# Performance work log

Measured on AMD Instinct MI355X. Metric: run time of the kernel, lower is better.

Reference implementation:

```python
import jax, jax.numpy as jnp
import numpy as np

N = 100_000      # nodes
E = 1_600_000    # edges (avg degree 16)
H = 4            # heads
C = 32           # per-head channels
HID = 128        # hidden = H*C
L = 4            # layers
IN, ED, OUT = 8, 6, 256
NEG_SLOPE = 0.2  # LeakyReLU default in GATv2Conv


def setup_inputs() -> dict:
    key = jax.random.key(0)
    ks = jax.random.split(key, 16)
    s = 0.1
    return {
        "x": jax.random.normal(ks[0], (N, IN), dtype=jnp.float32),
        "edge_index": jax.random.randint(ks[1], (2, E), 0, N, dtype=jnp.int32),
        "edge_attr": jax.random.normal(ks[2], (E, ED), dtype=jnp.float32),
        "W_in": jax.random.normal(ks[3], (IN, HID), dtype=jnp.float32) * s,
        "b_in": jnp.zeros((HID,), jnp.float32),
        "W_l": jax.random.normal(ks[4], (L, HID, HID), dtype=jnp.float32) * s,
        "b_l": jnp.zeros((L, HID), jnp.float32),
        "W_r": jax.random.normal(ks[5], (L, HID, HID), dtype=jnp.float32) * s,
        "b_r": jnp.zeros((L, HID), jnp.float32),
        "W_e": jax.random.normal(ks[6], (L, ED, HID), dtype=jnp.float32) * s,
        "att": jax.random.normal(ks[7], (L, H, C), dtype=jnp.float32) * s,
        "bias": jnp.zeros((L, HID), jnp.float32),
        "ln_w": jnp.ones((L, HID), jnp.float32),
        "ln_b": jnp.zeros((L, HID), jnp.float32),
        "W_out": jax.random.normal(ks[8], (HID, OUT), dtype=jnp.float32) * s,
        "b_out": jnp.zeros((OUT,), jnp.float32),
    }


def _elu(x):
    return jnp.where(x > 0, x, jnp.expm1(x))


def _leaky(x):
    return jnp.where(x > 0, x, NEG_SLOPE * x)


def _layernorm(x, w, b):
    mu = jnp.mean(x, axis=-1, keepdims=True)
    var = jnp.var(x, axis=-1, keepdims=True)
    return (x - mu) * jax.lax.rsqrt(var + 1e-5) * w + b


def _forward(x, edge_index, edge_attr, W_in, b_in, W_l, b_l, W_r, b_r,
             W_e, att, bias, ln_w, ln_b, W_out, b_out):
    src, dst = edge_index[0], edge_index[1]
    # add_self_loops with fill_value='mean': self-loop edge_attr = mean of incoming edge_attr
    deg = jax.ops.segment_sum(jnp.ones((E,), x.dtype), dst, num_segments=N)
    loop_attr = jax.ops.segment_sum(edge_attr, dst, num_segments=N) / jnp.maximum(deg, 1.0)[:, None]
    loops = jnp.arange(N, dtype=src.dtype)
    src_a = jnp.concatenate([src, loops])          # [E+N]
    dst_a = jnp.concatenate([dst, loops])          # [E+N]
    eattr_a = jnp.concatenate([edge_attr, loop_attr], axis=0)  # [E+N, ED]

    h = _elu(x @ W_in + b_in)  # [N, HID]
    for i in range(L):
        res = h
        xl = (h @ W_l[i] + b_l[i]).reshape(N, H, C)   # source transform
        xr = (h @ W_r[i] + b_r[i]).reshape(N, H, C)   # target transform
        ea = (eattr_a @ W_e[i]).reshape(-1, H, C)     # edge transform
        m = _leaky(xl[src_a] + xr[dst_a] + ea)        # [E+N, H, C]
        score = jnp.einsum('ehc,hc->eh', m, att[i])   # [E+N, H]
        # segment softmax over incoming edges per target node
        smax = jax.ops.segment_max(score, dst_a, num_segments=N)[dst_a]
        ex = jnp.exp(score - smax)
        denom = jax.ops.segment_sum(ex, dst_a, num_segments=N)[dst_a]
        alpha = ex / denom                             # [E+N, H]
        out = jax.ops.segment_sum(alpha[:, :, None] * xl[src_a], dst_a,
                                  num_segments=N).reshape(N, HID) + bias[i]
        h = _elu(_layernorm(out + res, ln_w[i], ln_b[i]))
        # dropout: identity (eval mode)
    return h @ W_out + b_out  # [N, OUT]


def reference(x, edge_index, edge_attr, W_in, b_in, W_l, b_l, W_r, b_r,
              W_e, att, bias, ln_w, ln_b, W_out, b_out):
    return _forward(x, edge_index, edge_attr, W_in, b_in, W_l, b_l, W_r, b_r,
                    W_e, att, bias, ln_w, ln_b, W_out, b_out)
```

## Files before the change

kernel.cpp:

```cpp
#include <hip/hip_runtime.h>
#include <hip/hip_bf16.h>
#include <hip/hip_fp16.h>

#define N_NODES 100000
#define N_EDGES 1600000
#define HEADS 4
#define CHN 32
#define HID 128
#define LAYERS 4
#define IN_F 8
#define ED_F 6
#define OUT_F 256
#define NEG_SLOPE 0.2f

typedef _Float16 f16x8 __attribute__((ext_vector_type(8)));
typedef _Float16 f16x4 __attribute__((ext_vector_type(4)));
typedef _Float16 h2 __attribute__((ext_vector_type(2)));
typedef float f32x4 __attribute__((ext_vector_type(4)));

#if defined(__has_builtin)
#if __has_builtin(__builtin_amdgcn_fdot2)
#define HAVE_FDOT2 1
#endif
#endif

__device__ __forceinline__ float elu_f(float x) {
    return x > 0.f ? x : expm1f(x);
}

__device__ __forceinline__ h2 bith2(float f) {
    union { float f; h2 h; } u; u.f = f; return u.h;
}

__device__ __forceinline__ float dot6(h2 e01, h2 e23, h2 e45, const h2* w) {
#ifdef HAVE_FDOT2
    return __builtin_amdgcn_fdot2(e45, w[2],
           __builtin_amdgcn_fdot2(e23, w[1],
           __builtin_amdgcn_fdot2(e01, w[0], 0.f, false), false), false);
#else
    float s = (float)e01[0] * (float)w[0][0];
    s = fmaf((float)e01[1], (float)w[0][1], s);
    s = fmaf((float)e23[0], (float)w[1][0], s);
    s = fmaf((float)e23[1], (float)w[1][1], s);
    s = fmaf((float)e45[0], (float)w[2][0], s);
    s = fmaf((float)e45[1], (float)w[2][1], s);
    return s;
#endif
}


__global__ void hist_kernel(const int* __restrict__ dst, int* __restrict__ fill) {
    int e = blockIdx.x * blockDim.x + threadIdx.x;
    if (e < N_EDGES) atomicAdd(&fill[dst[e]], 1);
}

__global__ void scan1_kernel(const int* __restrict__ cnt, int* __restrict__ bsum) {
    __shared__ int sd[256];
    int t = threadIdx.x;
    int base = blockIdx.x * 1024 + t * 4;
    int s = 0;
#pragma unroll
    for (int j = 0; j < 4; ++j) {
        int i = base + j;
        if (i < N_NODES) s += cnt[i];
    }
    sd[t] = s;
    for (int off = 128; off > 0; off >>= 1) {
        __syncthreads();
        if (t < off) sd[t] += sd[t + off];
    }
    if (t == 0) bsum[blockIdx.x] = sd[0];
}

__global__ void scan2_kernel(int* __restrict__ bsum, int* __restrict__ rowptr, int nb) {
    __shared__ int sd[256];
    int t = threadIdx.x;
    int v = (t < nb) ? bsum[t] : 0;
    sd[t] = v;
    __syncthreads();
    for (int off = 1; off < 256; off <<= 1) {
        int x = (t >= off) ? sd[t - off] : 0;
        __syncthreads();
        sd[t] += x;
        __syncthreads();
    }
    if (t < nb) bsum[t] = sd[t] - v;
    if (t == 0) rowptr[N_NODES] = sd[255];
}

__global__ void scan3_kernel(const int* __restrict__ cnt, const int* __restrict__ bsum,
                             int* __restrict__ rowptr) {
    __shared__ int sd[256];
    int t = threadIdx.x;
    int base = blockIdx.x * 1024 + t * 4;
    int v[4];
#pragma unroll
    for (int j = 0; j < 4; ++j) {
        int i = base + j;
        v[j] = (i < N_NODES) ? cnt[i] : 0;
    }
    int s = v[0] + v[1] + v[2] + v[3];
    sd[t] = s;
    __syncthreads();
    for (int off = 1; off < 256; off <<= 1) {
        int xv = (t >= off) ? sd[t - off] : 0;
        __syncthreads();
        sd[t] += xv;
        __syncthreads();
    }
    int excl = sd[t] - s + bsum[blockIdx.x];
    int pre = 0;
#pragma unroll
    for (int j = 0; j < 4; ++j) {
        int i = base + j;
        if (i < N_NODES) rowptr[i] = excl + pre;
        pre += v[j];
    }
}

__global__ void fill_kernel(const int* __restrict__ src, const int* __restrict__ dst,
                            const int* __restrict__ rowptr, int* __restrict__ fill,
                            int2* __restrict__ csr) {
    int e = blockIdx.x * blockDim.x + threadIdx.x;
    if (e >= N_EDGES) return;
    int d = dst[e];
    int p = rowptr[d] + atomicAdd(&fill[d], 1);
    csr[p] = make_int2(src[e] * (HID * 2), e * 16);
}

__global__ void ecvt_kernel(const float* __restrict__ eattr, __half* __restrict__ ea16) {
    int gid = blockIdx.x * blockDim.x + threadIdx.x;
    if (gid >= N_EDGES * 8) return;
    int e = gid >> 3, d = gid & 7;
    float v = (d < ED_F) ? eattr[e * ED_F + d] : 0.f;
    ea16[gid] = __float2half_rn(v);
}

__global__ void lattr_kernel(const int* __restrict__ rowptr, const int2* __restrict__ csr,
                             const float* __restrict__ eattr, __half* __restrict__ lat16) {
    int gid = blockIdx.x * blockDim.x + threadIdx.x;
    if (gid >= N_NODES * 8) return;
    int n = gid >> 3;
    int d = gid & 7;
    float s = 0.f;
    if (d < ED_F) {
        int rp0 = rowptr[n], rp1 = rowptr[n + 1];
        for (int p = rp0; p < rp1; ++p) {
            int eid = csr[p].y >> 4;
            s += eattr[(size_t)eid * ED_F + d];
        }
        int deg = rp1 - rp0;
        s /= (float)(deg > 0 ? deg : 1);
    }
    lat16[gid] = __float2half_rn(s);
}


__global__ void convw_kernel(const float* __restrict__ W_l, const float* __restrict__ W_r,
                             const float* __restrict__ W_out, __half* __restrict__ wbt) {
    int gid = blockIdx.x * blockDim.x + threadIdx.x;
    if (gid >= 5 * 256 * 128) return;
    int b = gid >> 15;
    int idx = gid & 32767;
    int n = idx >> 7, k = idx & 127;
    float val;
    if (b < 4)
        val = (n < HID) ? W_l[b * HID * HID + k * HID + n]
                        : W_r[b * HID * HID + k * HID + (n - HID)];
    else
        val = W_out[k * OUT_F + n];
    int boff = n * 256 + ((k * 2) ^ ((n & 7) << 4));
    *(__half*)((char*)wbt + (size_t)b * 65536 + boff) = __float2half_rn(val);
}


__global__ void in_kernel(const float* __restrict__ x, const float* __restrict__ Wi,
                          const float* __restrict__ bi, __half* __restrict__ h16) {
    int gid = blockIdx.x * blockDim.x + threadIdx.x;
    if (gid >= N_NODES * HID) return;
    int n = gid >> 7, j = gid & 127;
    float acc = bi[j];
#pragma unroll
    for (int k = 0; k < IN_F; ++k) acc = fmaf(x[n * IN_F + k], Wi[k * HID + j], acc);
    h16[gid] = __float2half_rn(elu_f(acc));
}


#define LDS_B_OFF 16384

template <int MODE>
__global__ __launch_bounds__(256, 2) void gemm_kernel(
    const __half* __restrict__ A16, const __half* __restrict__ Bt,
    const float* __restrict__ bias0, const float* __restrict__ bias1,
    __half* __restrict__ xl16, float* __restrict__ xr_out, float* __restrict__ outp) {
    __shared__ __align__(16) unsigned char smem[81920];
    int t = threadIdx.x;
    int row0 = blockIdx.x * 64;

#pragma unroll
    for (int it = 0; it < 4; ++it) {
        int idx = it * 256 + t;
        int r = idx >> 4;
        int kb = (idx & 15) * 16;
        f16x8 p = *(const f16x8*)((const char*)A16 + (size_t)(row0 + r) * 256 + kb);
        *(f16x8*)(smem + r * 256 + (kb ^ ((r & 7) << 4))) = p;
    }
#pragma unroll
    for (int it = 0; it < 16; ++it) {
        int off = (it * 256 + t) * 16;
        *(float4*)(smem + LDS_B_OFF + off) = *(const float4*)((const char*)Bt + off);
    }
    __syncthreads();

    int wave = t >> 6;
    int lane = t & 63;
    int lc = lane & 15, lr = lane >> 4;
    int cbase = wave * 64;

    f32x4 acc[4][4];
#pragma unroll
    for (int i = 0; i < 4; ++i)
#pragma unroll
        for (int j = 0; j < 4; ++j) acc[i][j] = (f32x4){0.f, 0.f, 0.f, 0.f};

#pragma unroll
    for (int kk = 0; kk < 4; ++kk) {
        int kb = kk * 64 + lr * 16;
        f16x8 av[4], bv[4];
#pragma unroll
        for (int rt = 0; rt < 4; ++rt) {
            int r = rt * 16 + lc;
            av[rt] = *(const f16x8*)(smem + r * 256 + (kb ^ ((r & 7) << 4)));
        }
#pragma unroll
        for (int ct = 0; ct < 4; ++ct) {
            int c = cbase + ct * 16 + lc;
            bv[ct] = *(const f16x8*)(smem + LDS_B_OFF + c * 256 + (kb ^ ((c & 7) << 4)));
        }
#pragma unroll
        for (int rt = 0; rt < 4; ++rt)
#pragma unroll
            for (int ct = 0; ct < 4; ++ct)
                acc[rt][ct] = __builtin_amdgcn_mfma_f32_16x16x32_f16(av[rt], bv[ct],
                                                                     acc[rt][ct], 0, 0, 0);
    }

#pragma unroll
    for (int ct = 0; ct < 4; ++ct) {
        int col = cbase + ct * 16 + lc;
        float bv;
        if (MODE == 0) bv = (col < HID) ? bias0[col] : bias1[col - HID];
        else bv = bias0[col];
#pragma unroll
        for (int rt = 0; rt < 4; ++rt) {
#pragma unroll
            for (int q = 0; q < 4; ++q) {
                int node = row0 + rt * 16 + lr * 4 + q;
                if (node < N_NODES) {
                    float val = acc[rt][ct][q] + bv;
                    if (MODE == 0) {
                        if (col < HID)
                            xl16[(size_t)node * HID + col] = __float2half_rn(val);
                        else
                            xr_out[(size_t)node * HID + (col - HID)] = val;
                    } else {
                        outp[(size_t)node * OUT_F + col] = val;
                    }
                }
            }
        }
    }
}


struct Slot {
    float4 er;
    float2 xv;
};

__device__ __forceinline__ void slot_issue(Slot& s, int i, int total, int rp0,
                                           const int2* __restrict__ csr,
                                           const char* eab, const char* lat16v,
                                           const char* xlb, int vbytes) {
    i = min(i, total - 1);
    const char* eb;
    const char* xb;
    if (i == 0) {
        eb = lat16v;
        xb = xlb + (size_t)vbytes;
    } else {
        int2 se = csr[rp0 + i - 1];
        eb = eab + (size_t)se.y;
        xb = xlb + (size_t)se.x;
    }
    s.er = *(const float4*)eb;
    s.xv = *(const float2*)xb;
}

__device__ __forceinline__ void slot_consume(const Slot& sl, int i, int total,
                                             const h2 we_h2[4][3], const float* attv,
                                             const float* xrv,
                                             float& denom, float* acc) {
    h2 e01 = bith2(sl.er.x), e23 = bith2(sl.er.y), e45 = bith2(sl.er.z);
    h2 x01 = bith2(sl.xv.x), x23 = bith2(sl.xv.y);
    float xf[4];
    xf[0] = (float)x01[0]; xf[1] = (float)x01[1];
    xf[2] = (float)x23[0]; xf[3] = (float)x23[1];
    float t = 0.f;
#pragma unroll
    for (int c = 0; c < 4; ++c) {
        float ea = dot6(e01, e23, e45, we_h2[c]);
        float m = xf[c] + xrv[c] + ea;
        m = m > 0.f ? m : NEG_SLOPE * m;
        t = fmaf(m, attv[c], t);
    }
    t += __shfl_xor(t, 1);
    t += __shfl_xor(t, 2);
    t += __shfl_xor(t, 4);
    float ex = __expf(t);
    ex = (i < total) ? ex : 0.f;
    denom += ex;
#pragma unroll
    for (int c = 0; c < 4; ++c) acc[c] = fmaf(ex, xf[c], acc[c]);
}

__global__ __launch_bounds__(64, 8) void edge_kernel(
    const __half* __restrict__ xl, const float* __restrict__ xr,
    __half* __restrict__ h16,
    const int* __restrict__ rowptr, const int2* __restrict__ csr,
    const __half* __restrict__ ea16, const __half* __restrict__ lat16,
    const float* __restrict__ We, const float* __restrict__ att,
    const float* __restrict__ bias_l, const float* __restrict__ lnw,
    const float* __restrict__ lnb) {
    int v = blockIdx.x;
    int lane = threadIdx.x;
    int half = lane >> 5;
    int hl = lane & 31;
    int c0 = hl * 4;

    h2 we_h2[4][3];
#pragma unroll
    for (int c = 0; c < 4; ++c)
#pragma unroll
        for (int d = 0; d < 3; ++d) {
            h2 w;
            w[0] = (_Float16)We[(2 * d) * HID + c0 + c];
            w[1] = (_Float16)We[(2 * d + 1) * HID + c0 + c];
            we_h2[c][d] = w;
        }
    float4 at4 = *(const float4*)(att + c0);
    float attv[4] = {at4.x, at4.y, at4.z, at4.w};
    float4 xr4 = *(const float4*)(xr + (size_t)v * HID + c0);
    float xrv[4] = {xr4.x, xr4.y, xr4.z, xr4.w};

    int rp0 = rowptr[v], rp1 = rowptr[v + 1];
    int total = (rp1 - rp0) + 1;
    int R = (total + 1) >> 1;

    const char* xlb = (const char*)xl + (size_t)c0 * 2;
    const char* eab = (const char*)ea16;
    const char* lat16v = (const char*)lat16 + (size_t)v * 16;
    int vbytes = v * (HID * 2);

    float denom = 0.f;
    float acc[4] = {0.f, 0.f, 0.f, 0.f};

    Slot sA, sB;
    slot_issue(sA, half, total, rp0, csr, eab, lat16v, xlb, vbytes);
    if (R > 1) slot_issue(sB, 2 + half, total, rp0, csr, eab, lat16v, xlb, vbytes);
    int r = 0;
    for (; r + 2 <= R; r += 2) {
        slot_consume(sA, 2 * r + half, total, we_h2, attv, xrv, denom, acc);
        if (r + 2 < R) slot_issue(sA, 2 * (r + 2) + half, total, rp0, csr, eab, lat16v, xlb, vbytes);
        slot_consume(sB, 2 * (r + 1) + half, total, we_h2, attv, xrv, denom, acc);
        if (r + 3 < R) slot_issue(sB, 2 * (r + 3) + half, total, rp0, csr, eab, lat16v, xlb, vbytes);
    }
    if (r < R) slot_consume(sA, 2 * r + half, total, we_h2, attv, xrv, denom, acc);

    denom += __shfl_xor(denom, 32);
#pragma unroll
    for (int c = 0; c < 4; ++c) acc[c] += __shfl_xor(acc[c], 32);

    float rd = 1.f / denom;

    float2 rb = *(const float2*)(h16 + (size_t)v * HID + c0);
    h2 r01 = bith2(rb.x), r23 = bith2(rb.y);
    float4 bv4 = *(const float4*)(bias_l + c0);
    float y[4];
    y[0] = acc[0] * rd + bv4.x + (float)r01[0];
    y[1] = acc[1] * rd + bv4.y + (float)r01[1];
    y[2] = acc[2] * rd + bv4.z + (float)r23[0];
    y[3] = acc[3] * rd + bv4.w + (float)r23[1];
    float s = y[0] + y[1] + y[2] + y[3];
    float sq = fmaf(y[0], y[0], fmaf(y[1], y[1], fmaf(y[2], y[2], y[3] * y[3])));
#pragma unroll
    for (int off = 1; off < 32; off <<= 1) {
        s += __shfl_xor(s, off);
        sq += __shfl_xor(sq, off);
    }
    float mu = s * (1.f / HID);
    float var = sq * (1.f / HID) - mu * mu;
    float rstd = rsqrtf(var + 1e-5f);
    float4 wv4 = *(const float4*)(lnw + c0);
    float4 lb4 = *(const float4*)(lnb + c0);
    if (half == 0) {
        f16x4 o;
        o[0] = (_Float16)elu_f((y[0] - mu) * rstd * wv4.x + lb4.x);
        o[1] = (_Float16)elu_f((y[1] - mu) * rstd * wv4.y + lb4.y);
        o[2] = (_Float16)elu_f((y[2] - mu) * rstd * wv4.z + lb4.z);
        o[3] = (_Float16)elu_f((y[3] - mu) * rstd * wv4.w + lb4.w);
        *(f16x4*)(h16 + (size_t)v * HID + c0) = o;
    }
}


extern "C" void kernel_launch(void* const* d_in, const int* in_sizes, int n_in,
                              void* d_out, int out_size, void* d_ws, size_t ws_size,
                              hipStream_t stream) {
    const float* x     = (const float*)d_in[0];
    const int*   ei    = (const int*)d_in[1];
    const float* eattr = (const float*)d_in[2];
    const float* W_in  = (const float*)d_in[3];
    const float* b_in  = (const float*)d_in[4];
    const float* W_l   = (const float*)d_in[5];
    const float* b_l   = (const float*)d_in[6];
    const float* W_r   = (const float*)d_in[7];
    const float* b_r   = (const float*)d_in[8];
    const float* W_e   = (const float*)d_in[9];
    const float* att   = (const float*)d_in[10];
    const float* bias  = (const float*)d_in[11];
    const float* lnw   = (const float*)d_in[12];
    const float* lnb   = (const float*)d_in[13];
    const float* W_out = (const float*)d_in[14];
    const float* b_out = (const float*)d_in[15];
    float* out = (float*)d_out;

    __half* h16   = (__half*)d_ws;
    __half* lat16 = h16 + (size_t)N_NODES * HID;
    int* rowptr   = (int*)(lat16 + (size_t)N_NODES * 8);
    int* fill     = rowptr + (N_NODES + 4);
    int2* csr     = (int2*)(fill + N_NODES);
    int* bsum     = (int*)(csr + N_EDGES);
    __half* wbt   = (__half*)(bsum + 256);

    float*  xr   = out;
    __half* xl   = (__half*)(out + (size_t)N_NODES * HID);
    __half* ea16 = xl + (size_t)N_NODES * HID;

    const int* srcv = ei;
    const int* dstv = ei + N_EDGES;

    hipMemsetAsync(fill, 0, N_NODES * sizeof(int), stream);
    hist_kernel<<<(N_EDGES + 255) / 256, 256, 0, stream>>>(dstv, fill);
    int nb = (N_NODES + 1023) / 1024;
    scan1_kernel<<<nb, 256, 0, stream>>>(fill, bsum);
    scan2_kernel<<<1, 256, 0, stream>>>(bsum, rowptr, nb);
    scan3_kernel<<<nb, 256, 0, stream>>>(fill, bsum, rowptr);
    hipMemsetAsync(fill, 0, N_NODES * sizeof(int), stream);
    fill_kernel<<<(N_EDGES + 255) / 256, 256, 0, stream>>>(srcv, dstv, rowptr, fill, csr);
    ecvt_kernel<<<(N_EDGES * 8 + 255) / 256, 256, 0, stream>>>(eattr, ea16);
    lattr_kernel<<<(N_NODES * 8 + 255) / 256, 256, 0, stream>>>(rowptr, csr, eattr, lat16);

    convw_kernel<<<(5 * 256 * 128 + 255) / 256, 256, 0, stream>>>(W_l, W_r, W_out, wbt);
    in_kernel<<<(N_NODES * HID) / 256, 256, 0, stream>>>(x, W_in, b_in, h16);

    int gemm_grid = (N_NODES + 63) / 64;
    for (int l = 0; l < LAYERS; ++l) {
        gemm_kernel<0><<<gemm_grid, 256, 0, stream>>>(
            h16, wbt + (size_t)l * 32768, b_l + (size_t)l * HID, b_r + (size_t)l * HID,
            xl, xr, nullptr);
        edge_kernel<<<N_NODES, 64, 0, stream>>>(
            xl, xr, h16, rowptr, csr, ea16, lat16,
            W_e + (size_t)l * ED_F * HID, att + (size_t)l * HEADS * CHN,
            bias + (size_t)l * HID, lnw + (size_t)l * HID, lnb + (size_t)l * HID);
    }

    gemm_kernel<1><<<gemm_grid, 256, 0, stream>>>(
        h16, wbt + (size_t)4 * 32768, b_out, nullptr, nullptr, nullptr, out);
}
```

Before: 1.063 ms.

## Interleave xl/xr as fp16 rows, persistent GEMM grid, lattr from fp16 edges

Stores the target transform xr in fp16 next to xl in one 256-wide row per node, so the edge kernel reads xr from the same row as xl and does half the bytes for xr. The GEMM becomes a persistent grid of 512 blocks that load the weight matrix into LDS once and loop over row tiles, instead of reloading weights in every one of about 1563 blocks. The loop-attribute kernel now reads the padded fp16 edge attributes instead of fp32. In exchange, xr loses precision, and the wider row stride for xl gathers can reduce cache locality.

Result: faster. 925.4 us (-12.9%).

```diff
diff --git a/kernel.cpp b/kernel.cpp
--- a/kernel.cpp
+++ b/kernel.cpp
@@ -12,6 +12,9 @@
 #define ED_F 6
 #define OUT_F 256
 #define NEG_SLOPE 0.2f
+
+#define NT_GEMM ((N_NODES + 63) / 64)
+#define GRID_GEMM 512
 
 typedef _Float16 f16x8 __attribute__((ext_vector_type(8)));
 typedef _Float16 f16x4 __attribute__((ext_vector_type(4)));
@@ -125,7 +128,7 @@
     if (e >= N_EDGES) return;
     int d = dst[e];
     int p = rowptr[d] + atomicAdd(&fill[d], 1);
-    csr[p] = make_int2(src[e] * (HID * 2), e * 16);
+    csr[p] = make_int2(src[e] * 512, e * 16);
 }
 
 __global__ void ecvt_kernel(const float* __restrict__ eattr, __half* __restrict__ ea16) {
@@ -137,7 +140,7 @@
 }
 
 __global__ void lattr_kernel(const int* __restrict__ rowptr, const int2* __restrict__ csr,
-                             const float* __restrict__ eattr, __half* __restrict__ lat16) {
+                             const __half* __restrict__ ea16, __half* __restrict__ lat16) {
     int gid = blockIdx.x * blockDim.x + threadIdx.x;
     if (gid >= N_NODES * 8) return;
     int n = gid >> 3;
@@ -147,7 +150,7 @@
         int rp0 = rowptr[n], rp1 = rowptr[n + 1];
         for (int p = rp0; p < rp1; ++p) {
             int eid = csr[p].y >> 4;
-            s += eattr[(size_t)eid * ED_F + d];
+            s += (float)ea16[(size_t)eid * 8 + d];
         }
         int deg = rp1 - rp0;
         s /= (float)(deg > 0 ? deg : 1);
@@ -192,79 +195,79 @@
 __global__ __launch_bounds__(256, 2) void gemm_kernel(
     const __half* __restrict__ A16, const __half* __restrict__ Bt,
     const float* __restrict__ bias0, const float* __restrict__ bias1,
-    __half* __restrict__ xl16, float* __restrict__ xr_out, float* __restrict__ outp) {
+    __half* __restrict__ xlr16, float* __restrict__ outp) {
     __shared__ __align__(16) unsigned char smem[81920];
     int t = threadIdx.x;
-    int row0 = blockIdx.x * 64;
-
-#pragma unroll
-    for (int it = 0; it < 4; ++it) {
-        int idx = it * 256 + t;
-        int r = idx >> 4;
-        int kb = (idx & 15) * 16;
-        f16x8 p = *(const f16x8*)((const char*)A16 + (size_t)(row0 + r) * 256 + kb);
-        *(f16x8*)(smem + r * 256 + (kb ^ ((r & 7) << 4))) = p;
-    }
+
 #pragma unroll
     for (int it = 0; it < 16; ++it) {
         int off = (it * 256 + t) * 16;
         *(float4*)(smem + LDS_B_OFF + off) = *(const float4*)((const char*)Bt + off);
     }
-    __syncthreads();
 
     int wave = t >> 6;
     int lane = t & 63;
     int lc = lane & 15, lr = lane >> 4;
     int cbase = wave * 64;
 
-    f32x4 acc[4][4];
-#pragma unroll
-    for (int i = 0; i < 4; ++i)
-#pragma unroll
-        for (int j = 0; j < 4; ++j) acc[i][j] = (f32x4){0.f, 0.f, 0.f, 0.f};
-
-#pragma unroll
-    for (int kk = 0; kk < 4; ++kk) {
-        int kb = kk * 64 + lr * 16;
-        f16x8 av[4], bv[4];
-#pragma unroll
-        for (int rt = 0; rt < 4; ++rt) {
-            int r = rt * 16 + lc;
-            av[rt] = *(const f16x8*)(smem + r * 256 + (kb ^ ((r & 7) << 4)));
+    for (int tile = blockIdx.x; tile < NT_GEMM; tile += GRID_GEMM) {
+        int row0 = tile * 64;
+#pragma unroll
+        for (int it = 0; it < 4; ++it) {
+            int idx = it * 256 + t;
+            int r = idx >> 4;
+            int kb = (idx & 15) * 16;
+            f16x8 p = *(const f16x8*)((const char*)A16 + (size_t)(row0 + r) * 256 + kb);
+            *(f16x8*)(smem + r * 256 + (kb ^ ((r & 7) << 4))) = p;
         }
+        __syncthreads();
+
+        f32x4 acc[4][4];
+#pragma unroll
+        for (int i = 0; i < 4; ++i)
+#pragma unroll
+            for (int j = 0; j < 4; ++j) acc[i][j] = (f32x4){0.f, 0.f, 0.f, 0.f};
+
+#pragma unroll
+        for (int kk = 0; kk < 4; ++kk) {
+            int kb = kk * 64 + lr * 16;
+            f16x8 av[4], bv[4];
+#pragma unroll
+            for (int rt = 0; rt < 4; ++rt) {
+                int r = rt * 16 + lc;
+                av[rt] = *(const f16x8*)(smem + r * 256 + (kb ^ ((r & 7) << 4)));
+            }
+#pragma unroll
+            for (int ct = 0; ct < 4; ++ct) {
+                int c = cbase + ct * 16 + lc;
+                bv[ct] = *(const f16x8*)(smem + LDS_B_OFF + c * 256 + (kb ^ ((c & 7) << 4)));
+            }
+#pragma unroll
+            for (int rt = 0; rt < 4; ++rt)
+#pragma unroll
+                for (int ct = 0; ct < 4; ++ct)
+                    acc[rt][ct] = __builtin_amdgcn_mfma_f32_16x16x32_f16(av[rt], bv[ct],
+                                                                         acc[rt][ct], 0, 0, 0);
+        }
+        __syncthreads();
+
 #pragma unroll
         for (int ct = 0; ct < 4; ++ct) {
-            int c = cbase + ct * 16 + lc;
-            bv[ct] = *(const f16x8*)(smem + LDS_B_OFF + c * 256 + (kb ^ ((c & 7) << 4)));
-        }
-#pragma unroll
-        for (int rt = 0; rt < 4; ++rt)
-#pragma unroll
-            for (int ct = 0; ct < 4; ++ct)
-                acc[rt][ct] = __builtin_amdgcn_mfma_f32_16x16x32_f16(av[rt], bv[ct],
-                                                                     acc[rt][ct], 0, 0, 0);
-    }
-
-#pragma unroll
-    for (int ct = 0; ct < 4; ++ct) {
-        int col = cbase + ct * 16 + lc;
-        float bv;
-        if (MODE == 0) bv = (col < HID) ? bias0[col] : bias1[col - HID];
-        else bv = bias0[col];
-#pragma unroll
-        for (int rt = 0; rt < 4; ++rt) {
-#pragma unroll
-            for (int q = 0; q < 4; ++q) {
-                int node = row0 + rt * 16 + lr * 4 + q;
-                if (node < N_NODES) {
-                    float val = acc[rt][ct][q] + bv;
-                    if (MODE == 0) {
-                        if (col < HID)
-                            xl16[(size_t)node * HID + col] = __float2half_rn(val);
+            int col = cbase + ct * 16 + lc;
+            float bv;
+            if (MODE == 0) bv = (col < HID) ? bias0[col] : bias1[col - HID];
+            else bv = bias0[col];
+#pragma unroll
+            for (int rt = 0; rt < 4; ++rt) {
+#pragma unroll
+                for (int q = 0; q < 4; ++q) {
+                    int node = row0 + rt * 16 + lr * 4 + q;
+                    if (node < N_NODES) {
+                        float val = acc[rt][ct][q] + bv;
+                        if (MODE == 0)
+                            xlr16[(size_t)node * 256 + col] = __float2half_rn(val);
                         else
-                            xr_out[(size_t)node * HID + (col - HID)] = val;
-                    } else {
-                        outp[(size_t)node * OUT_F + col] = val;
+                            outp[(size_t)node * OUT_F + col] = val;
                     }
                 }
             }
@@ -325,7 +328,7 @@
 }
 
 __global__ __launch_bounds__(64, 8) void edge_kernel(
-    const __half* __restrict__ xl, const float* __restrict__ xr,
+    const __half* __restrict__ xlr16,
     __half* __restrict__ h16,
     const int* __restrict__ rowptr, const int2* __restrict__ csr,
     const __half* __restrict__ ea16, const __half* __restrict__ lat16,
@@ -350,17 +353,22 @@
         }
     float4 at4 = *(const float4*)(att + c0);
     float attv[4] = {at4.x, at4.y, at4.z, at4.w};
-    float4 xr4 = *(const float4*)(xr + (size_t)v * HID + c0);
-    float xrv[4] = {xr4.x, xr4.y, xr4.z, xr4.w};
+    float xrv[4];
+    {
+        float2 xraw = *(const float2*)(xlr16 + (size_t)v * 256 + 128 + c0);
+        h2 xr01 = bith2(xraw.x), xr23 = bith2(xraw.y);
+        xrv[0] = (float)xr01[0]; xrv[1] = (float)xr01[1];
+        xrv[2] = (float)xr23[0]; xrv[3] = (float)xr23[1];
+    }
 
     int rp0 = rowptr[v], rp1 = rowptr[v + 1];
     int total = (rp1 - rp0) + 1;
     int R = (total + 1) >> 1;
 
-    const char* xlb = (const char*)xl + (size_t)c0 * 2;
+    const char* xlb = (const char*)xlr16 + (size_t)c0 * 2;
     const char* eab = (const char*)ea16;
     const char* lat16v = (const char*)lat16 + (size_t)v * 16;
-    int vbytes = v * (HID * 2);
+    int vbytes = v * 512;
 
     float denom = 0.f;
     float acc[4] = {0.f, 0.f, 0.f, 0.f};
@@ -443,9 +451,8 @@
     int* bsum     = (int*)(csr + N_EDGES);
     __half* wbt   = (__half*)(bsum + 256);
 
-    float*  xr   = out;
-    __half* xl   = (__half*)(out + (size_t)N_NODES * HID);
-    __half* ea16 = xl + (size_t)N_NODES * HID;
+    __half* xlr16 = (__half*)out;
+    __half* ea16  = xlr16 + (size_t)N_NODES * 256;
 
     const int* srcv = ei;
     const int* dstv = ei + N_EDGES;
@@ -459,22 +466,21 @@
     hipMemsetAsync(fill, 0, N_NODES * sizeof(int), stream);
     fill_kernel<<<(N_EDGES + 255) / 256, 256, 0, stream>>>(srcv, dstv, rowptr, fill, csr);
     ecvt_kernel<<<(N_EDGES * 8 + 255) / 256, 256, 0, stream>>>(eattr, ea16);
-    lattr_kernel<<<(N_NODES * 8 + 255) / 256, 256, 0, stream>>>(rowptr, csr, eattr, lat16);
+    lattr_kernel<<<(N_NODES * 8 + 255) / 256, 256, 0, stream>>>(rowptr, csr, ea16, lat16);
 
     convw_kernel<<<(5 * 256 * 128 + 255) / 256, 256, 0, stream>>>(W_l, W_r, W_out, wbt);
     in_kernel<<<(N_NODES * HID) / 256, 256, 0, stream>>>(x, W_in, b_in, h16);
 
-    int gemm_grid = (N_NODES + 63) / 64;
     for (int l = 0; l < LAYERS; ++l) {
-        gemm_kernel<0><<<gemm_grid, 256, 0, stream>>>(
+        gemm_kernel<0><<<GRID_GEMM, 256, 0, stream>>>(
             h16, wbt + (size_t)l * 32768, b_l + (size_t)l * HID, b_r + (size_t)l * HID,
-            xl, xr, nullptr);
+            xlr16, nullptr);
         edge_kernel<<<N_NODES, 64, 0, stream>>>(
-            xl, xr, h16, rowptr, csr, ea16, lat16,
+            xlr16, h16, rowptr, csr, ea16, lat16,
             W_e + (size_t)l * ED_F * HID, att + (size_t)l * HEADS * CHN,
             bias + (size_t)l * HID, lnw + (size_t)l * HID, lnb + (size_t)l * HID);
     }
 
-    gemm_kernel<1><<<gemm_grid, 256, 0, stream>>>(
-        h16, wbt + (size_t)4 * 32768, b_out, nullptr, nullptr, nullptr, out);
-}
+    gemm_kernel<1><<<GRID_GEMM, 256, 0, stream>>>(
+        h16, wbt + (size_t)4 * 32768, b_out, nullptr, nullptr, out);
+}
```
